# Kernel optimization log

Measured on AMD Instinct MI355X. Metric: run time of the kernel, lower is better.

The kernel has to match this reference:

```python
import jax, jax.numpy as jnp
import numpy as np

BATCH, T, N = 8, 2048, 512


def setup_inputs() -> dict:
    key = jax.random.key(0)
    ks = jax.random.split(key, 8)
    scale = 1.0 / np.sqrt(2.0 * (N + N) / 2.0) / np.sqrt(2.0)  # GlorotNormal / sqrt(2)
    u = jax.random.normal(ks[0], (BATCH, T, N), dtype=jnp.float32)
    C_re = jax.random.normal(ks[1], (N, N), dtype=jnp.float32) * scale
    C_im = jax.random.normal(ks[2], (N, N), dtype=jnp.float32) * scale
    B_re = jax.random.normal(ks[3], (N, N), dtype=jnp.float32) * scale
    B_im = jax.random.normal(ks[4], (N, N), dtype=jnp.float32) * scale
    D = jax.random.normal(ks[5], (N,), dtype=jnp.float32)
    # nu drawn from the numerically-stable end of [log(-log rmax), log(-log rmin)]
    nu = jax.random.uniform(ks[6], (N,), minval=-4.6, maxval=-3.7, dtype=jnp.float32)
    theta = jax.random.uniform(ks[7], (N,), minval=0.0, maxval=3.14 / 10, dtype=jnp.float32)
    # gamma initialized as sqrt(1 - |lambda|^2), lambda = exp(-exp(nu) + i*theta)
    gamma = jnp.sqrt(1.0 - jnp.exp(-2.0 * jnp.exp(nu)))
    return {"u": u, "C_re": C_re, "C_im": C_im, "B_re": B_re, "B_im": B_im,
            "D": D, "nu": nu, "theta": theta, "gamma": gamma}


def reference(u, C_re, C_im, B_re, B_im, D, nu, theta, gamma):
    # log_lambda = -exp(nu) + i*theta  (the TF code names this `lambda_`)
    log_lam = (-jnp.exp(nu)).astype(jnp.complex64) + 1j * theta.astype(jnp.complex64)  # (n,)
    t = jnp.arange(u.shape[1], dtype=jnp.float32).astype(jnp.complex64)[:, None]       # (T,1)
    lam_pow = jnp.exp(log_lam[None, :] * t)    # (T,n) == diag(Lambda^t)
    lam_minpow = jnp.exp(-log_lam[None, :] * t)  # (T,n) == diag(Lambda^-t)
    Bm = (B_re + 1j * B_im).astype(jnp.complex64)  # (n,n)
    Cm = (C_re + 1j * C_im).astype(jnp.complex64)  # (n,n)
    # new_u = (gamma * u) @ B   (complex)
    new_u = (gamma * u).astype(jnp.complex64) @ Bm  # (b,t,n)
    # diag einsums in the original are elementwise multiplies
    x = jnp.cumsum(new_u * lam_minpow[None], axis=1) * lam_pow[None]  # (b,t,n)
    y = jnp.real(x @ Cm) + D * u
    return y
```

## Files before the change

### kernel.cpp

```cpp
#include <hip/hip_runtime.h>
#include <hip/hip_bf16.h>
#include <math.h>
#include <stdint.h>

#define BATCH 8
#define T_LEN 2048
#define NDIM 512
#define M_ROWS (BATCH * T_LEN)
#define CHUNK 32
#define NCHUNK (T_LEN / CHUNK)


typedef __attribute__((ext_vector_type(8))) short bf16x8;
typedef __attribute__((ext_vector_type(4))) float floatx4;

#define VMWAIT(n) asm volatile("s_waitcnt vmcnt(" #n ")" ::: "memory")

__device__ __forceinline__ unsigned short f2bf(float f) {
    union { float f; unsigned u; } v; v.f = f;
    unsigned r = v.u + 0x7fff + ((v.u >> 16) & 1);
    return (unsigned short)(r >> 16);
}
__device__ __forceinline__ float bf2f(unsigned short h) {
    union { unsigned u; float f; } v; v.u = ((unsigned)h) << 16;
    return v.f;
}
__device__ __forceinline__ float bf2f_lo(unsigned u) {
    union { unsigned u; float f; } v; v.u = u << 16; return v.f;
}
__device__ __forceinline__ float bf2f_hi(unsigned u) {
    union { unsigned u; float f; } v; v.u = u & 0xffff0000u; return v.f;
}

__device__ __forceinline__ void gld_lds16(const unsigned short* g, unsigned short* l) {
    __builtin_amdgcn_global_load_lds(
        (const __attribute__((address_space(1))) unsigned int*)(uintptr_t)g,
        (__attribute__((address_space(3))) unsigned int*)(uintptr_t)l,
        16, 0, 0);
}

__global__ __launch_bounds__(256) void k_prep(
    const float* __restrict__ u,
    const float* __restrict__ Bre, const float* __restrict__ Bim,
    const float* __restrict__ Cre, const float* __restrict__ Cim,
    const float* __restrict__ gamma,
    unsigned short* __restrict__ ubf,
    unsigned short* __restrict__ BT, unsigned short* __restrict__ CT)
{
    __shared__ unsigned short tile[32][33];
    const int blk = blockIdx.x;
    if (blk < 4096) {
        size_t i = ((size_t)blk * 256 + threadIdx.x) * 8;
        float4 a = *(const float4*)&u[i];
        float4 b = *(const float4*)&u[i + 4];
        ushort4 p0, p1;
        p0.x = f2bf(a.x); p0.y = f2bf(a.y); p0.z = f2bf(a.z); p0.w = f2bf(a.w);
        p1.x = f2bf(b.x); p1.y = f2bf(b.y); p1.z = f2bf(b.z); p1.w = f2bf(b.w);
        *(ushort4*)&ubf[i] = p0;
        *(ushort4*)&ubf[i + 4] = p1;
        return;
    }
    const int p = blk - 4096;
    const int z = p >> 8;
    const int rem = p & 255;
    const int n0 = (rem & 15) * 32, k0 = (rem >> 4) * 32;
    const float* __restrict__ src = (z == 0) ? Bre : (z == 1) ? Bim : (z == 2) ? Cre : Cim;
    const int tx = threadIdx.x & 31, ty = threadIdx.x >> 5;

#pragma unroll
    for (int j = 0; j < 4; ++j) {
        int k = k0 + ty + j * 8;
        float s = (z < 2) ? gamma[k] : (z == 3 ? -1.f : 1.f);
        tile[ty + j * 8][tx] = f2bf(s * src[(size_t)k * NDIM + n0 + tx]);
    }
    __syncthreads();
#pragma unroll
    for (int j = 0; j < 4; ++j) {
        int n = n0 + ty + j * 8;
        unsigned short v = tile[tx][ty + j * 8];
        if (z == 0) {
            int row = ((n >> 6) << 7) + (n & 63);
            BT[(size_t)row * 512 + k0 + tx] = v;
        } else if (z == 1) {
            int row = ((n >> 6) << 7) + 64 + (n & 63);
            BT[(size_t)row * 512 + k0 + tx] = v;
        } else if (z == 2) {
            int k = k0 + tx;
            int col = ((k >> 6) << 7) + (k & 63);
            CT[(size_t)n * 1024 + col] = v;
        } else {
            int k = k0 + tx;
            int col = ((k >> 6) << 7) + 64 + (k & 63);
            CT[(size_t)n * 1024 + col] = v;
        }
    }
}

__global__ __launch_bounds__(256) void k_gemm_in(
    const unsigned short* __restrict__ A,
    const unsigned short* __restrict__ BT,
    const float* __restrict__ nu, const float* __restrict__ theta,
    unsigned short* __restrict__ X,
    float* __restrict__ carry)
{
    __shared__ unsigned short smem[24576];

    const int tid = threadIdx.x;
    const int w = tid >> 6, l = tid & 63;
    const int bm = blockIdx.x * 128;
    const int bn = blockIdx.y * 128;
    const int wm = (w & 1) * 64, wn = (w >> 1) * 64;
    const int lm = l & 15, lq = l >> 4;
    const int srow = w * 16 + (l >> 2);
    const int scol = (l & 3) * 8;

    floatx4 acc[4][4];
#pragma unroll
    for (int i = 0; i < 4; ++i)
#pragma unroll
        for (int j = 0; j < 4; ++j) acc[i][j] = (floatx4)0.f;

    auto STAGE = [&](int buf, int t) {
        unsigned short* as = &smem[buf * 8192];
        unsigned short* bs = as + 4096;
        const int k0 = t * 32;
        gld_lds16(&A[(size_t)(bm + srow) * 512 + k0 + scol],       &as[srow * 32 + scol]);
        gld_lds16(&A[(size_t)(bm + 64 + srow) * 512 + k0 + scol],  &as[(64 + srow) * 32 + scol]);
        gld_lds16(&BT[(size_t)(bn + srow) * 512 + k0 + scol],      &bs[srow * 32 + scol]);
        gld_lds16(&BT[(size_t)(bn + 64 + srow) * 512 + k0 + scol], &bs[(64 + srow) * 32 + scol]);
    };
    auto COMPUTE = [&](int buf) {
        const unsigned short* as = &smem[buf * 8192];
        const unsigned short* bs = as + 4096;
        bf16x8 af[4], bfr[4];
#pragma unroll
        for (int i = 0; i < 4; ++i)
            af[i] = *(const bf16x8*)&as[(wm + i * 16 + lm) * 32 + lq * 8];
#pragma unroll
        for (int j = 0; j < 4; ++j)
            bfr[j] = *(const bf16x8*)&bs[(wn + j * 16 + lm) * 32 + lq * 8];
#pragma unroll
        for (int i = 0; i < 4; ++i)
#pragma unroll
            for (int j = 0; j < 4; ++j)
                acc[i][j] = __builtin_amdgcn_mfma_f32_16x16x32_bf16(af[i], bfr[j], acc[i][j], 0, 0, 0);
    };

    STAGE(0, 0);
    STAGE(1, 1);
#pragma unroll
    for (int t = 0; t < 14; ++t) {
        STAGE((t + 2) % 3, t + 2);
        VMWAIT(8);
        __builtin_amdgcn_s_barrier();
        __builtin_amdgcn_sched_barrier(0);
        COMPUTE(t % 3);
        __builtin_amdgcn_sched_barrier(0);
        __builtin_amdgcn_s_barrier();
    }
    VMWAIT(4);
    __builtin_amdgcn_s_barrier();
    __builtin_amdgcn_sched_barrier(0);
    COMPUTE(2);
    __builtin_amdgcn_sched_barrier(0);
    __builtin_amdgcn_s_barrier();
    VMWAIT(0);
    __builtin_amdgcn_s_barrier();
    __builtin_amdgcn_sched_barrier(0);
    COMPUTE(0);

    __syncthreads();
#pragma unroll
    for (int i = 0; i < 4; ++i)
#pragma unroll
        for (int j = 0; j < 4; ++j) {
            int col = wn + j * 16 + lm;
#pragma unroll
            for (int r = 0; r < 4; ++r) {
                int row = wm + i * 16 + lq * 4 + r;
                unsigned short v = f2bf(acc[i][j][r]);
                smem[row * 128 + col] = v;
                X[(size_t)(bm + row) * 1024 + bn + col] = v;
            }
        }
    __syncthreads();
    {
        const int chunk = tid >> 6;
        const int ch = tid & 63;
        const int n = (bn >> 1) + ch;
        const float rr = __expf(-__expf(nu[n]));
        const float lre = rr * __cosf(theta[n]);
        const float lim = rr * __sinf(theta[n]);
        const unsigned short* base = &smem[chunk * 32 * 128 + ch];
        float xre = 0.f, xim = 0.f;
#pragma unroll 8
        for (int t = 0; t < 32; ++t) {
            float ure = bf2f(base[t * 128]);
            float uim = bf2f(base[t * 128 + 64]);
            float a = lre * xre - lim * xim + ure;
            float b = lre * xim + lim * xre + uim;
            xre = a; xim = b;
        }
        const int bb = bm >> 11;
        const int cg = ((bm & 2047) >> 5) + chunk;
        size_t ci = ((size_t)bb * NCHUNK + cg) * NDIM + n;
        *(float2*)&carry[ci * 2] = make_float2(xre, xim);
    }
}

__global__ __launch_bounds__(256) void k_scan_apply(
    unsigned short* __restrict__ X,
    const float* __restrict__ nu, const float* __restrict__ theta,
    const float* __restrict__ carry)
{
    const int t2 = threadIdx.x;
    const int n0 = 2 * t2;
    const int b = blockIdx.x >> 6, c = blockIdx.x & 63;
    const float ex0 = __expf(nu[n0]), ex1 = __expf(nu[n0 + 1]);
    const float r0 = __expf(-ex0), r1 = __expf(-ex1);
    const float lre0 = r0 * __cosf(theta[n0]),     lim0 = r0 * __sinf(theta[n0]);
    const float lre1 = r1 * __cosf(theta[n0 + 1]), lim1 = r1 * __sinf(theta[n0 + 1]);
    const float rc0 = expf(-ex0 * (float)CHUNK), rc1 = expf(-ex1 * (float)CHUNK);
    const float th0 = theta[n0] * (float)CHUNK,  th1 = theta[n0 + 1] * (float)CHUNK;
    const float A0 = rc0 * cosf(th0), B0 = rc0 * sinf(th0);
    const float A1 = rc1 * cosf(th1), B1 = rc1 * sinf(th1);

    float xre0 = 0.f, xim0 = 0.f, xre1 = 0.f, xim1 = 0.f;
    for (int cc = 0; cc < c; ++cc) {
        size_t idx = ((size_t)b * NCHUNK + cc) * NDIM + n0;
        float4 cv = *(const float4*)&carry[idx * 2];
        float a0 = A0 * xre0 - B0 * xim0 + cv.x;
        float b0 = A0 * xim0 + B0 * xre0 + cv.y;
        float a1 = A1 * xre1 - B1 * xim1 + cv.z;
        float b1 = A1 * xim1 + B1 * xre1 + cv.w;
        xre0 = a0; xim0 = b0; xre1 = a1; xim1 = b1;
    }

    const int recol = ((n0 >> 6) << 7) + (n0 & 63);
    size_t m = (size_t)b * T_LEN + (size_t)c * CHUNK;
#pragma unroll 8
    for (int t = 0; t < CHUNK; ++t, ++m) {
        unsigned re = *(const unsigned*)&X[m * 1024 + recol];
        unsigned im = *(const unsigned*)&X[m * 1024 + recol + 64];
        float u0 = bf2f_lo(re), u1 = bf2f_hi(re);
        float v0 = bf2f_lo(im), v1 = bf2f_hi(im);
        float a0 = lre0 * xre0 - lim0 * xim0 + u0;
        float b0 = lre0 * xim0 + lim0 * xre0 + v0;
        float a1 = lre1 * xre1 - lim1 * xim1 + u1;
        float b1 = lre1 * xim1 + lim1 * xre1 + v1;
        xre0 = a0; xim0 = b0; xre1 = a1; xim1 = b1;
        unsigned pr = (unsigned)f2bf(xre0) | ((unsigned)f2bf(xre1) << 16);
        unsigned pim = (unsigned)f2bf(xim0) | ((unsigned)f2bf(xim1) << 16);
        *(unsigned*)&X[m * 1024 + recol] = pr;
        *(unsigned*)&X[m * 1024 + recol + 64] = pim;
    }
}

__global__ __launch_bounds__(256) void k_gemm_out(
    const unsigned short* __restrict__ Xbf,
    const unsigned short* __restrict__ CT,
    const float* __restrict__ D,
    const unsigned short* __restrict__ Ubf,
    float* __restrict__ Y)
{
    __shared__ unsigned short smem[32768];

    const int tid = threadIdx.x;
    const int w = tid >> 6, l = tid & 63;
    const int bm = blockIdx.x * 128;
    const int bn = blockIdx.y * 128;
    const int wm = (w & 1) * 64, wn = (w >> 1) * 64;
    const int lm = l & 15, lq = l >> 4;
    const int srow = w * 16 + (l >> 2);
    const int scol = (l & 3) * 8;

    floatx4 acc[4][4];
#pragma unroll
    for (int i = 0; i < 4; ++i)
#pragma unroll
        for (int j = 0; j < 4; ++j) acc[i][j] = (floatx4)0.f;

    auto STAGE = [&](int buf, int t) {
        unsigned short* as = &smem[buf * 8192];
        unsigned short* bs = as + 4096;
        const int k0 = t * 32;
        gld_lds16(&Xbf[(size_t)(bm + srow) * 1024 + k0 + scol],      &as[srow * 32 + scol]);
        gld_lds16(&Xbf[(size_t)(bm + 64 + srow) * 1024 + k0 + scol], &as[(64 + srow) * 32 + scol]);
        gld_lds16(&CT[(size_t)(bn + srow) * 1024 + k0 + scol],       &bs[srow * 32 + scol]);
        gld_lds16(&CT[(size_t)(bn + 64 + srow) * 1024 + k0 + scol],  &bs[(64 + srow) * 32 + scol]);
    };
    auto COMPUTE = [&](int buf) {
        const unsigned short* as = &smem[buf * 8192];
        const unsigned short* bs = as + 4096;
        bf16x8 af[4], bfr[4];
#pragma unroll
        for (int i = 0; i < 4; ++i)
            af[i] = *(const bf16x8*)&as[(wm + i * 16 + lm) * 32 + lq * 8];
#pragma unroll
        for (int j = 0; j < 4; ++j)
            bfr[j] = *(const bf16x8*)&bs[(wn + j * 16 + lm) * 32 + lq * 8];
#pragma unroll
        for (int i = 0; i < 4; ++i)
#pragma unroll
            for (int j = 0; j < 4; ++j)
                acc[i][j] = __builtin_amdgcn_mfma_f32_16x16x32_bf16(af[i], bfr[j], acc[i][j], 0, 0, 0);
    };

    STAGE(0, 0);
    STAGE(1, 1);
    STAGE(2, 2);
#pragma unroll
    for (int t = 0; t < 29; ++t) {
        STAGE((t + 3) & 3, t + 3);
        VMWAIT(12);
        __builtin_amdgcn_s_barrier();
        __builtin_amdgcn_sched_barrier(0);
        COMPUTE(t & 3);
        __builtin_amdgcn_sched_barrier(0);
        __builtin_amdgcn_s_barrier();
    }
    VMWAIT(8);
    __builtin_amdgcn_s_barrier();
    __builtin_amdgcn_sched_barrier(0);
    COMPUTE(1);
    __builtin_amdgcn_sched_barrier(0);
    __builtin_amdgcn_s_barrier();
    VMWAIT(4);
    __builtin_amdgcn_s_barrier();
    __builtin_amdgcn_sched_barrier(0);
    COMPUTE(2);
    __builtin_amdgcn_sched_barrier(0);
    __builtin_amdgcn_s_barrier();
    VMWAIT(0);
    __builtin_amdgcn_s_barrier();
    __builtin_amdgcn_sched_barrier(0);
    COMPUTE(3);

#pragma unroll
    for (int i = 0; i < 4; ++i)
#pragma unroll
        for (int j = 0; j < 4; ++j) {
            int col = bn + wn + j * 16 + lm;
            float dv = D[col];
#pragma unroll
            for (int r = 0; r < 4; ++r) {
                int row = bm + wm + i * 16 + lq * 4 + r;
                size_t off = (size_t)row * NDIM + col;
                Y[off] = acc[i][j][r] + dv * bf2f(Ubf[off]);
            }
        }
}

extern "C" void kernel_launch(void* const* d_in, const int* in_sizes, int n_in,
                              void* d_out, int out_size, void* d_ws, size_t ws_size,
                              hipStream_t stream)
{
    const float* u     = (const float*)d_in[0];
    const float* C_re  = (const float*)d_in[1];
    const float* C_im  = (const float*)d_in[2];
    const float* B_re  = (const float*)d_in[3];
    const float* B_im  = (const float*)d_in[4];
    const float* D     = (const float*)d_in[5];
    const float* nu    = (const float*)d_in[6];
    const float* theta = (const float*)d_in[7];
    const float* gamma = (const float*)d_in[8];
    float* y = (float*)d_out;

    unsigned short* X   = (unsigned short*)d_ws;
    unsigned short* ubf = X + (size_t)M_ROWS * 1024;
    unsigned short* BT  = ubf + (size_t)M_ROWS * 512;
    unsigned short* CT  = BT + (size_t)1024 * 512;
    float* carry = (float*)(CT + (size_t)512 * 1024);

    k_prep<<<4096 + 1024, 256, 0, stream>>>(u, B_re, B_im, C_re, C_im, gamma, ubf, BT, CT);
    k_gemm_in<<<dim3(M_ROWS / 128, 8), 256, 0, stream>>>(ubf, BT, nu, theta, X, carry);
    k_scan_apply<<<BATCH * NCHUNK, 256, 0, stream>>>(X, nu, theta, carry);
    k_gemm_out<<<dim3(M_ROWS / 128, 4), 256, 0, stream>>>(X, CT, D, ubf, y);
}
```

Measured before the change: 172.6 us.

## Enlarge GEMM tiles to 256 rows with 512 threads, K=64 stages and XOR-swizzled LDS

Both GEMM kernels move from 128x128 tiles with 256 threads to 256-row tiles with 512 threads. The input GEMM now uses a 256x256 tile with 8x4 accumulators per wave. Each stage now loads K=64 instead of 32 into LDS with an XOR swizzle to avoid bank conflicts, and the pipeline drops from 3-4 buffers to double buffering. The in-kernel chunk carry scan is reworked to cover 128 channels per block, with two passes per thread. The aim is more data reuse per global load and fewer barriers, at the cost of higher register and LDS use, lower occupancy, a shallower prefetch and fewer blocks.

Measured after the change: 168.6 us. 2.4% less time.

```diff
diff --git a/kernel.cpp b/kernel.cpp
--- a/kernel.cpp
+++ b/kernel.cpp
@@ -96,107 +96,115 @@
     }
 }
 
-__global__ __launch_bounds__(256) void k_gemm_in(
+__global__ __launch_bounds__(512) void k_gemm_in(
     const unsigned short* __restrict__ A,
     const unsigned short* __restrict__ BT,
     const float* __restrict__ nu, const float* __restrict__ theta,
     unsigned short* __restrict__ X,
     float* __restrict__ carry)
 {
-    __shared__ unsigned short smem[24576];
+    __shared__ unsigned short smem[65536];
 
     const int tid = threadIdx.x;
     const int w = tid >> 6, l = tid & 63;
-    const int bm = blockIdx.x * 128;
-    const int bn = blockIdx.y * 128;
-    const int wm = (w & 1) * 64, wn = (w >> 1) * 64;
+    const int bm = blockIdx.x * 256;
+    const int bn = blockIdx.y * 256;
+    const int wm = (w & 1) * 128, wn = (w >> 1) * 64;
     const int lm = l & 15, lq = l >> 4;
-    const int srow = w * 16 + (l >> 2);
-    const int scol = (l & 3) * 8;
-
-    floatx4 acc[4][4];
-#pragma unroll
-    for (int i = 0; i < 4; ++i)
+    const int sr = tid >> 3;
+    const int scw = ((tid & 7) ^ (sr & 7)) * 8;
+    const int scl = (tid & 7) * 8;
+    const int rsw = (lm & 7) << 3;
+
+    floatx4 acc[8][4];
+#pragma unroll
+    for (int i = 0; i < 8; ++i)
 #pragma unroll
         for (int j = 0; j < 4; ++j) acc[i][j] = (floatx4)0.f;
 
     auto STAGE = [&](int buf, int t) {
-        unsigned short* as = &smem[buf * 8192];
-        unsigned short* bs = as + 4096;
-        const int k0 = t * 32;
-        gld_lds16(&A[(size_t)(bm + srow) * 512 + k0 + scol],       &as[srow * 32 + scol]);
-        gld_lds16(&A[(size_t)(bm + 64 + srow) * 512 + k0 + scol],  &as[(64 + srow) * 32 + scol]);
-        gld_lds16(&BT[(size_t)(bn + srow) * 512 + k0 + scol],      &bs[srow * 32 + scol]);
-        gld_lds16(&BT[(size_t)(bn + 64 + srow) * 512 + k0 + scol], &bs[(64 + srow) * 32 + scol]);
+        unsigned short* as = &smem[buf * 32768];
+        unsigned short* bs = as + 16384;
+        const int k0 = t * 64;
+#pragma unroll
+        for (int o = 0; o < 4; ++o)
+            gld_lds16(&A[(size_t)(bm + o * 64 + sr) * 512 + k0 + scw],
+                      &as[(o * 64 + sr) * 64 + scl]);
+#pragma unroll
+        for (int o = 0; o < 4; ++o)
+            gld_lds16(&BT[(size_t)(bn + o * 64 + sr) * 512 + k0 + scw],
+                      &bs[(o * 64 + sr) * 64 + scl]);
     };
     auto COMPUTE = [&](int buf) {
-        const unsigned short* as = &smem[buf * 8192];
-        const unsigned short* bs = as + 4096;
-        bf16x8 af[4], bfr[4];
-#pragma unroll
-        for (int i = 0; i < 4; ++i)
-            af[i] = *(const bf16x8*)&as[(wm + i * 16 + lm) * 32 + lq * 8];
-#pragma unroll
-        for (int j = 0; j < 4; ++j)
-            bfr[j] = *(const bf16x8*)&bs[(wn + j * 16 + lm) * 32 + lq * 8];
-#pragma unroll
-        for (int i = 0; i < 4; ++i)
+        const unsigned short* as = &smem[buf * 32768];
+        const unsigned short* bs = as + 16384;
+#pragma unroll
+        for (int ks = 0; ks < 2; ++ks) {
+            const int co = ((ks * 32 + lq * 8) ^ rsw);
+            bf16x8 af[8], bfr[4];
+#pragma unroll
+            for (int i = 0; i < 8; ++i)
+                af[i] = *(const bf16x8*)&as[(wm + i * 16 + lm) * 64 + co];
 #pragma unroll
             for (int j = 0; j < 4; ++j)
-                acc[i][j] = __builtin_amdgcn_mfma_f32_16x16x32_bf16(af[i], bfr[j], acc[i][j], 0, 0, 0);
+                bfr[j] = *(const bf16x8*)&bs[(wn + j * 16 + lm) * 64 + co];
+#pragma unroll
+            for (int i = 0; i < 8; ++i)
+#pragma unroll
+                for (int j = 0; j < 4; ++j)
+                    acc[i][j] = __builtin_amdgcn_mfma_f32_16x16x32_bf16(af[i], bfr[j], acc[i][j], 0, 0, 0);
+        }
     };
 
     STAGE(0, 0);
-    STAGE(1, 1);
-#pragma unroll
-    for (int t = 0; t < 14; ++t) {
-        STAGE((t + 2) % 3, t + 2);
+#pragma unroll
+    for (int t = 0; t < 7; ++t) {
+        STAGE((t + 1) & 1, t + 1);
         VMWAIT(8);
         __builtin_amdgcn_s_barrier();
         __builtin_amdgcn_sched_barrier(0);
-        COMPUTE(t % 3);
+        COMPUTE(t & 1);
         __builtin_amdgcn_sched_barrier(0);
         __builtin_amdgcn_s_barrier();
-    }
-    VMWAIT(4);
-    __builtin_amdgcn_s_barrier();
-    __builtin_amdgcn_sched_barrier(0);
-    COMPUTE(2);
-    __builtin_amdgcn_sched_barrier(0);
-    __builtin_amdgcn_s_barrier();
+        __builtin_amdgcn_sched_barrier(0);
+    }
     VMWAIT(0);
     __builtin_amdgcn_s_barrier();
     __builtin_amdgcn_sched_barrier(0);
-    COMPUTE(0);
+    COMPUTE(1);
 
     __syncthreads();
 #pragma unroll
-    for (int i = 0; i < 4; ++i)
+    for (int i = 0; i < 8; ++i)
 #pragma unroll
         for (int j = 0; j < 4; ++j) {
-            int col = wn + j * 16 + lm;
+            int lcol = wn + j * 16 + lm;
 #pragma unroll
             for (int r = 0; r < 4; ++r) {
-                int row = wm + i * 16 + lq * 4 + r;
+                int lrow = wm + i * 16 + lq * 4 + r;
                 unsigned short v = f2bf(acc[i][j][r]);
-                smem[row * 128 + col] = v;
-                X[(size_t)(bm + row) * 1024 + bn + col] = v;
+                smem[lrow * 256 + lcol] = v;
+                X[(size_t)(bm + lrow) * 1024 + bn + lcol] = v;
             }
         }
     __syncthreads();
-    {
-        const int chunk = tid >> 6;
-        const int ch = tid & 63;
+#pragma unroll
+    for (int q = 0; q < 2; ++q) {
+        const int s = tid + q * 512;
+        const int chunk = s >> 7;
+        const int ch = s & 127;
         const int n = (bn >> 1) + ch;
+        const int gl = ch >> 6, cc = ch & 63;
+        const int recol = gl * 128 + cc;
         const float rr = __expf(-__expf(nu[n]));
         const float lre = rr * __cosf(theta[n]);
         const float lim = rr * __sinf(theta[n]);
-        const unsigned short* base = &smem[chunk * 32 * 128 + ch];
+        const unsigned short* base = &smem[chunk * 32 * 256 + recol];
         float xre = 0.f, xim = 0.f;
 #pragma unroll 8
         for (int t = 0; t < 32; ++t) {
-            float ure = bf2f(base[t * 128]);
-            float uim = bf2f(base[t * 128 + 64]);
+            float ure = bf2f(base[t * 256]);
+            float uim = bf2f(base[t * 256 + 64]);
             float a = lre * xre - lim * xim + ure;
             float b = lre * xim + lim * xre + uim;
             xre = a; xim = b;
@@ -256,23 +264,25 @@
     }
 }
 
-__global__ __launch_bounds__(256) void k_gemm_out(
+__global__ __launch_bounds__(512) void k_gemm_out(
     const unsigned short* __restrict__ Xbf,
     const unsigned short* __restrict__ CT,
     const float* __restrict__ D,
     const unsigned short* __restrict__ Ubf,
     float* __restrict__ Y)
 {
-    __shared__ unsigned short smem[32768];
+    __shared__ unsigned short smem[49152];
 
     const int tid = threadIdx.x;
     const int w = tid >> 6, l = tid & 63;
-    const int bm = blockIdx.x * 128;
+    const int bm = blockIdx.x * 256;
     const int bn = blockIdx.y * 128;
-    const int wm = (w & 1) * 64, wn = (w >> 1) * 64;
+    const int wm = (w & 3) * 64, wn = (w >> 2) * 64;
     const int lm = l & 15, lq = l >> 4;
-    const int srow = w * 16 + (l >> 2);
-    const int scol = (l & 3) * 8;
+    const int sr = tid >> 3;
+    const int scw = ((tid & 7) ^ (sr & 7)) * 8;
+    const int scl = (tid & 7) * 8;
+    const int rsw = (lm & 7) << 3;
 
     floatx4 acc[4][4];
 #pragma unroll
@@ -281,60 +291,55 @@
         for (int j = 0; j < 4; ++j) acc[i][j] = (floatx4)0.f;
 
     auto STAGE = [&](int buf, int t) {
-        unsigned short* as = &smem[buf * 8192];
-        unsigned short* bs = as + 4096;
-        const int k0 = t * 32;
-        gld_lds16(&Xbf[(size_t)(bm + srow) * 1024 + k0 + scol],      &as[srow * 32 + scol]);
-        gld_lds16(&Xbf[(size_t)(bm + 64 + srow) * 1024 + k0 + scol], &as[(64 + srow) * 32 + scol]);
-        gld_lds16(&CT[(size_t)(bn + srow) * 1024 + k0 + scol],       &bs[srow * 32 + scol]);
-        gld_lds16(&CT[(size_t)(bn + 64 + srow) * 1024 + k0 + scol],  &bs[(64 + srow) * 32 + scol]);
+        unsigned short* as = &smem[buf * 24576];
+        unsigned short* bs = as + 16384;
+        const int k0 = t * 64;
+#pragma unroll
+        for (int o = 0; o < 4; ++o)
+            gld_lds16(&Xbf[(size_t)(bm + o * 64 + sr) * 1024 + k0 + scw],
+                      &as[(o * 64 + sr) * 64 + scl]);
+#pragma unroll
+        for (int o = 0; o < 2; ++o)
+            gld_lds16(&CT[(size_t)(bn + o * 64 + sr) * 1024 + k0 + scw],
+                      &bs[(o * 64 + sr) * 64 + scl]);
     };
     auto COMPUTE = [&](int buf) {
-        const unsigned short* as = &smem[buf * 8192];
-        const unsigned short* bs = as + 4096;
-        bf16x8 af[4], bfr[4];
-#pragma unroll
-        for (int i = 0; i < 4; ++i)
-            af[i] = *(const bf16x8*)&as[(wm + i * 16 + lm) * 32 + lq * 8];
-#pragma unroll
-        for (int j = 0; j < 4; ++j)
-            bfr[j] = *(const bf16x8*)&bs[(wn + j * 16 + lm) * 32 + lq * 8];
-#pragma unroll
-        for (int i = 0; i < 4; ++i)
+        const unsigned short* as = &smem[buf * 24576];
+        const unsigned short* bs = as + 16384;
+#pragma unroll
+        for (int ks = 0; ks < 2; ++ks) {
+            const int co = ((ks * 32 + lq * 8) ^ rsw);
+            bf16x8 af[4], bfr[4];
+#pragma unroll
+            for (int i = 0; i < 4; ++i)
+                af[i] = *(const bf16x8*)&as[(wm + i * 16 + lm) * 64 + co];
 #pragma unroll
             for (int j = 0; j < 4; ++j)
-                acc[i][j] = __builtin_amdgcn_mfma_f32_16x16x32_bf16(af[i], bfr[j], acc[i][j], 0, 0, 0);
+                bfr[j] = *(const bf16x8*)&bs[(wn + j * 16 + lm) * 64 + co];
+#pragma unroll
+            for (int i = 0; i < 4; ++i)
+#pragma unroll
+                for (int j = 0; j < 4; ++j)
+                    acc[i][j] = __builtin_amdgcn_mfma_f32_16x16x32_bf16(af[i], bfr[j], acc[i][j], 0, 0, 0);
+        }
     };
 
     STAGE(0, 0);
-    STAGE(1, 1);
-    STAGE(2, 2);
-#pragma unroll
-    for (int t = 0; t < 29; ++t) {
-        STAGE((t + 3) & 3, t + 3);
-        VMWAIT(12);
+#pragma unroll
+    for (int t = 0; t < 15; ++t) {
+        STAGE((t + 1) & 1, t + 1);
+        VMWAIT(6);
         __builtin_amdgcn_s_barrier();
         __builtin_amdgcn_sched_barrier(0);
-        COMPUTE(t & 3);
+        COMPUTE(t & 1);
         __builtin_amdgcn_sched_barrier(0);
         __builtin_amdgcn_s_barrier();
-    }
-    VMWAIT(8);
+        __builtin_amdgcn_sched_barrier(0);
+    }
+    VMWAIT(0);
     __builtin_amdgcn_s_barrier();
     __builtin_amdgcn_sched_barrier(0);
     COMPUTE(1);
-    __builtin_amdgcn_sched_barrier(0);
-    __builtin_amdgcn_s_barrier();
-    VMWAIT(4);
-    __builtin_amdgcn_s_barrier();
-    __builtin_amdgcn_sched_barrier(0);
-    COMPUTE(2);
-    __builtin_amdgcn_sched_barrier(0);
-    __builtin_amdgcn_s_barrier();
-    VMWAIT(0);
-    __builtin_amdgcn_s_barrier();
-    __builtin_amdgcn_sched_barrier(0);
-    COMPUTE(3);
 
 #pragma unroll
     for (int i = 0; i < 4; ++i)
@@ -373,7 +378,7 @@
     float* carry = (float*)(CT + (size_t)512 * 1024);
 
     k_prep<<<4096 + 1024, 256, 0, stream>>>(u, B_re, B_im, C_re, C_im, gamma, ubf, BT, CT);
-    k_gemm_in<<<dim3(M_ROWS / 128, 8), 256, 0, stream>>>(ubf, BT, nu, theta, X, carry);
+    k_gemm_in<<<dim3(M_ROWS / 256, 4), 512, 0, stream>>>(ubf, BT, nu, theta, X, carry);
     k_scan_apply<<<BATCH * NCHUNK, 256, 0, stream>>>(X, nu, theta, carry);
-    k_gemm_out<<<dim3(M_ROWS / 128, 4), 256, 0, stream>>>(X, CT, D, ubf, y);
-}
+    k_gemm_out<<<dim3(M_ROWS / 256, 4), 512, 0, stream>>>(X, CT, D, ubf, y);
+}
```
